# Kernel tuning notes

Measured on AMD Instinct MI355X. Metric: run time of the kernel, lower is better.

## Reference

```python
import jax, jax.numpy as jnp
import numpy as np

MAX_SEQ_LENGTH = 32
LN_EPS = 1e-5


def setup_inputs() -> dict:
    key = jax.random.key(0)
    ks = jax.random.split(key, 6)
    N, T, D, H, O = 256, 1024, 128, 256, 128
    G = 4 * H
    # torch kaiming_normal_ on a 2D (in, 4H) tensor: fan_in = size(1) = 4H, std = sqrt(2/fan_in)
    std_k = float(np.sqrt(2.0 / G))
    X = jax.random.normal(ks[0], (N, T, D), dtype=jnp.float32)
    Wx = jax.random.normal(ks[1], (D, G), dtype=jnp.float32) * std_k
    Wh = jax.random.normal(ks[2], (H, G), dtype=jnp.float32) * std_k
    b = jnp.zeros((G,), dtype=jnp.float32)
    W1 = jax.random.normal(ks[3], (H, H), dtype=jnp.float32) * float(np.sqrt(1.0 / H))
    b1 = jnp.zeros((H,), dtype=jnp.float32)
    ln_gamma = jnp.ones((H,), dtype=jnp.float32)
    ln_beta = jnp.zeros((H,), dtype=jnp.float32)
    W2 = jax.random.normal(ks[4], (H, O), dtype=jnp.float32) * float(np.sqrt(1.0 / H))
    b2 = jnp.zeros((O,), dtype=jnp.float32)
    return {"X": X, "Wx": Wx, "Wh": Wh, "b": b, "W1": W1, "b1": b1,
            "ln_gamma": ln_gamma, "ln_beta": ln_beta, "W2": W2, "b2": b2}


def _fc(h, W1, b1, ln_gamma, ln_beta, W2, b2):
    z = h @ W1 + b1
    mu = jnp.mean(z, axis=-1, keepdims=True)
    var = jnp.var(z, axis=-1, keepdims=True)
    z = (z - mu) * jax.lax.rsqrt(var + LN_EPS) * ln_gamma + ln_beta
    z = jax.nn.relu(z)
    return z @ W2 + b2


def reference(X, Wx, Wh, b, W1, b1, ln_gamma, ln_beta, W2, b2):
    N, T, D = X.shape
    H = Wh.shape[0]
    h0 = jnp.zeros((N, H), dtype=X.dtype)
    c0 = jnp.zeros((N, H), dtype=X.dtype)

    # --- encoder: standard LSTM cell (sigmoid/tanh gates) ---
    def enc_step(carry, x_t):
        h, c = carry
        fm = x_t @ Wx + h @ Wh + b  # (N, 4H)
        i = jax.nn.sigmoid(fm[:, 0:H])
        f = jax.nn.sigmoid(fm[:, H:2 * H])
        o = jax.nn.sigmoid(fm[:, 2 * H:3 * H])
        g = jnp.tanh(fm[:, 3 * H:4 * H])
        c = c * f + i * g
        h = o * jnp.tanh(c)
        return (h, c), None

    (h, c), _ = jax.lax.scan(enc_step, (h0, c0), jnp.swapaxes(X, 0, 1))

    # --- decoder: NOTE original code uses RAW gate slices (no sigmoid/tanh),
    # and start_token is zeros so the start_token @ Wx term is exactly 0. ---
    def dec_step(carry, _):
        h, c = carry
        fm = h @ Wh + b  # zeros @ Wx contributes 0
        i = fm[:, 0:H]
        f = fm[:, H:2 * H]
        o = fm[:, 2 * H:3 * H]
        g = fm[:, 3 * H:4 * H]
        c = c * f + i * g
        h = o * jnp.tanh(c)
        y = _fc(h, W1, b1, ln_gamma, ln_beta, W2, b2)
        return (h, c), y

    _, ys = jax.lax.scan(dec_step, (h, c), None, length=MAX_SEQ_LENGTH)
    return jnp.swapaxes(ys, 0, 1)  # (N, max_seq_length, output_dim)
```

## Files before the change

kernel.cpp:

```cpp
#include <hip/hip_runtime.h>
#include <cmath>

typedef _Float16 f16;
typedef _Float16 f16x4v __attribute__((ext_vector_type(4)));
typedef _Float16 f16x8v __attribute__((ext_vector_type(8)));
typedef float f32x4v __attribute__((ext_vector_type(4)));

#define NTHR 256
#define WPG  16

__device__ __forceinline__ float sigmoidf_(float x) { return 1.0f / (1.0f + expf(-x)); }

__device__ __forceinline__ void store_sc(float* p, float v) {
  asm volatile("global_store_dword %0, %1, off sc0 sc1" :: "v"(p), "v"(v) : "memory");
}

__device__ __forceinline__ void ld4_sc(const float* p,
                                       float4& a, float4& b, float4& c, float4& d) {
  asm volatile(
      "global_load_dwordx4 %0, %4, off sc0 sc1\n\t"
      "global_load_dwordx4 %1, %5, off sc0 sc1\n\t"
      "global_load_dwordx4 %2, %6, off sc0 sc1\n\t"
      "global_load_dwordx4 %3, %7, off sc0 sc1\n\t"
      "s_waitcnt vmcnt(0)"
      : "=&v"(a), "=&v"(b), "=&v"(c), "=&v"(d)
      : "v"(p), "v"(p + 1024), "v"(p + 2048), "v"(p + 3072)
      : "memory");
}

__device__ __forceinline__ void arrive_bar(unsigned* cg) {
  asm volatile("s_waitcnt vmcnt(0)" ::: "memory");
  __syncthreads();
  if (threadIdx.x == 0)
    (void)__hip_atomic_fetch_add(cg, 1u, __ATOMIC_RELAXED, __HIP_MEMORY_SCOPE_AGENT);
}

__device__ __forceinline__ void wait_bar(unsigned* cg, unsigned target) {
  if (threadIdx.x == 0) {
    unsigned guard = 0;
    while (__hip_atomic_load(cg, __ATOMIC_RELAXED, __HIP_MEMORY_SCOPE_AGENT) < target) {
      __builtin_amdgcn_s_sleep(1);
      if (++guard > (1u << 22)) break;
    }
  }
  __syncthreads();
}

__device__ __forceinline__ void conv4_wr(float4 v, f16* ph, f16* pl) {
  f16x4v h, l;
  h[0] = (f16)v.x; h[1] = (f16)v.y; h[2] = (f16)v.z; h[3] = (f16)v.w;
  l[0] = (f16)(v.x - (float)h[0]); l[1] = (f16)(v.y - (float)h[1]);
  l[2] = (f16)(v.z - (float)h[2]); l[3] = (f16)(v.w - (float)h[3]);
  *(f16x4v*)ph = h; *(f16x4v*)pl = l;
}

__device__ __forceinline__ void conv8_wr(float4 a, float4 b, f16* ph, f16* pl) {
  f16x8v h, l;
  h[0]=(f16)a.x; h[1]=(f16)a.y; h[2]=(f16)a.z; h[3]=(f16)a.w;
  h[4]=(f16)b.x; h[5]=(f16)b.y; h[6]=(f16)b.z; h[7]=(f16)b.w;
  l[0]=(f16)(a.x-(float)h[0]); l[1]=(f16)(a.y-(float)h[1]);
  l[2]=(f16)(a.z-(float)h[2]); l[3]=(f16)(a.w-(float)h[3]);
  l[4]=(f16)(b.x-(float)h[4]); l[5]=(f16)(b.y-(float)h[5]);
  l[6]=(f16)(b.z-(float)h[6]); l[7]=(f16)(b.w-(float)h[7]);
  *(f16x8v*)ph = h; *(f16x8v*)pl = l;
}

__global__ __launch_bounds__(NTHR, 1) void lstm_k(
    const float* __restrict__ X,  const float* __restrict__ Wx,
    const float* __restrict__ Wh, const float* __restrict__ Bg,
    const float* __restrict__ W1, const float* __restrict__ B1,
    const float* __restrict__ LNG, const float* __restrict__ LNB,
    const float* __restrict__ W2, const float* __restrict__ B2,
    float* __restrict__ Y, unsigned* __restrict__ CNT,
    float* __restrict__ hbuf, float* __restrict__ zbuf)
{
  __shared__ f16   A_hi[16][392];
  __shared__ f16   A_lo[16][392];
  __shared__ float fm_lds[16][65];
  __shared__ float hst[16][264];
  __shared__ float w1_lds[16][268];
  __shared__ float w2_lds[8][268];
  __shared__ float lng_lds[256], lnb_lds[256];
  __shared__ float ln_mu[16], ln_rs[16];

  const int tid = threadIdx.x;
  const int wg  = blockIdx.x;
  const int g   = wg & 15;
  const int jm  = wg >> 4;
  const int n0  = g * 16;
  const int k0  = jm * 16;
  unsigned* cg  = CNT + g * 32;

  const int l     = tid & 63;
  const int w     = __builtin_amdgcn_readfirstlane(tid >> 6);
  const int krow0 = (l >> 4) * 8;
  const int arow  = l & 15;

  f16x8v Bh[12], Bl[12];
  {
    const int bcol = w * 256 + k0 + (l & 15);
    #pragma unroll
    for (int kt = 0; kt < 12; ++kt) {
      #pragma unroll
      for (int j = 0; j < 8; ++j) {
        int k = kt * 32 + krow0 + j;
        float v = (kt < 4) ? Wx[k * 1024 + bcol] : Wh[(k - 128) * 1024 + bcol];
        f16 hi = (f16)v;
        Bh[kt][j] = hi;
        Bl[kt][j] = (f16)(v - (float)hi);
      }
    }
  }

  for (int idx = tid; idx < 256 * 16; idx += NTHR) {
    int k = idx >> 4, cc = idx & 15;
    w1_lds[cc][k] = W1[k * 256 + k0 + cc];
  }
  for (int idx = tid; idx < 256 * 8; idx += NTHR) {
    int k = idx >> 3, cc = idx & 7;
    w2_lds[cc][k] = W2[k * 128 + jm * 8 + cc];
  }
  lng_lds[tid] = LNG[tid];
  lnb_lds[tid] = LNB[tid];

  const int gr = tid >> 4, gk = tid & 15;
  const float bias0 = Bg[      k0 + gk];
  const float bias1 = Bg[256 + k0 + gk];
  const float bias2 = Bg[512 + k0 + gk];
  const float bias3 = Bg[768 + k0 + gk];
  const float b1reg = B1[k0 + gk];
  const float b2reg = (tid < 128) ? B2[jm * 8 + (tid & 7)] : 0.0f;
  float c_reg = 0.0f;

  {
    const float* xp = X + (size_t)(n0 + (tid >> 4)) * 131072 + (size_t)(tid & 15) * 8;
    float4 xa = *(const float4*)xp;
    float4 xb = *(const float4*)(xp + 4);
    conv8_wr(xa, xb, &A_hi[tid >> 4][(tid & 15) * 8], &A_lo[tid >> 4][(tid & 15) * 8]);
    f16x8v z8 = {0,0,0,0,0,0,0,0};
    *(f16x8v*)&A_hi[tid >> 4][128 + (tid & 15) * 16] = z8;
    *(f16x8v*)&A_hi[tid >> 4][136 + (tid & 15) * 16] = z8;
    *(f16x8v*)&A_lo[tid >> 4][128 + (tid & 15) * 16] = z8;
    *(f16x8v*)&A_lo[tid >> 4][136 + (tid & 15) * 16] = z8;
  }
  __syncthreads();

  auto stage_h_A = [&](const float* hs) {
    float4 v0, v1, v2, v3;
    ld4_sc(hs, v0, v1, v2, v3);
    conv4_wr(v0, &A_hi[w     ][128 + 4 * l], &A_lo[w     ][128 + 4 * l]);
    conv4_wr(v1, &A_hi[w + 4 ][128 + 4 * l], &A_lo[w + 4 ][128 + 4 * l]);
    conv4_wr(v2, &A_hi[w + 8 ][128 + 4 * l], &A_lo[w + 8 ][128 + 4 * l]);
    conv4_wr(v3, &A_hi[w + 12][128 + 4 * l], &A_lo[w + 12][128 + 4 * l]);
  };

  for (int t = 0; t < 1024; ++t) {
    float4 xa, xb;
    if (t < 1023) {
      const float* xp = X + (size_t)(n0 + (tid >> 4)) * 131072
                          + (size_t)(t + 1) * 128 + (size_t)(tid & 15) * 8;
      xa = *(const float4*)xp;
      xb = *(const float4*)(xp + 4);
    }

    f16x8v ah[12], al[12];
    {
      const f16* pah = &A_hi[arow][krow0];
      const f16* pal = &A_lo[arow][krow0];
      #pragma unroll
      for (int kt = 0; kt < 12; ++kt) {
        ah[kt] = *(const f16x8v*)(pah + kt * 32);
        al[kt] = *(const f16x8v*)(pal + kt * 32);
      }
    }
    f32x4v ac0 = {0,0,0,0}, ac1 = {0,0,0,0}, ac2 = {0,0,0,0};
    #pragma unroll
    for (int kt = 0; kt < 12; ++kt) {
      ac0 = __builtin_amdgcn_mfma_f32_16x16x32_f16(ah[kt], Bh[kt], ac0, 0, 0, 0);
      ac1 = __builtin_amdgcn_mfma_f32_16x16x32_f16(ah[kt], Bl[kt], ac1, 0, 0, 0);
      ac2 = __builtin_amdgcn_mfma_f32_16x16x32_f16(al[kt], Bh[kt], ac2, 0, 0, 0);
    }
    #pragma unroll
    for (int q = 0; q < 4; ++q)
      fm_lds[(l >> 4) * 4 + q][w * 16 + (l & 15)] = ac0[q] + ac1[q] + ac2[q];
    __syncthreads();

    {
      float fi = fm_lds[gr][     gk] + bias0;
      float ff = fm_lds[gr][16 + gk] + bias1;
      float fo = fm_lds[gr][32 + gk] + bias2;
      float fg = fm_lds[gr][48 + gk] + bias3;
      float si = sigmoidf_(fi), sf = sigmoidf_(ff), so = sigmoidf_(fo);
      float tg = tanhf(fg);
      c_reg = c_reg * sf + si * tg;
      float hv = so * tanhf(c_reg);
      store_sc(hbuf + (size_t)(t & 1) * 65536 + (size_t)(n0 + gr) * 256 + k0 + gk, hv);
    }

    if (t < 1023)
      conv8_wr(xa, xb, &A_hi[tid >> 4][(tid & 15) * 8], &A_lo[tid >> 4][(tid & 15) * 8]);

    arrive_bar(cg);
    if (t < 1023) {
      wait_bar(cg, (unsigned)(WPG * (t + 1)));
      stage_h_A(hbuf + (size_t)(t & 1) * 65536 + (size_t)n0 * 256 + (size_t)tid * 4);
      __syncthreads();
    }
  }

  wait_bar(cg, (unsigned)(WPG * 1024));
  stage_h_A(hbuf + (size_t)65536  + (size_t)n0 * 256 + (size_t)tid * 4);
  __syncthreads();
  unsigned arr = 1024;

  for (int s = 0; s < 32; ++s) {
    const int t = 1024 + s;

    f16x8v ah[8], al[8];
    {
      const f16* pah = &A_hi[arow][128 + krow0];
      const f16* pal = &A_lo[arow][128 + krow0];
      #pragma unroll
      for (int kt = 0; kt < 8; ++kt) {
        ah[kt] = *(const f16x8v*)(pah + kt * 32);
        al[kt] = *(const f16x8v*)(pal + kt * 32);
      }
    }
    f32x4v ac0 = {0,0,0,0}, ac1 = {0,0,0,0}, ac2 = {0,0,0,0};
    #pragma unroll
    for (int kt = 0; kt < 8; ++kt) {
      ac0 = __builtin_amdgcn_mfma_f32_16x16x32_f16(ah[kt], Bh[kt + 4], ac0, 0, 0, 0);
      ac1 = __builtin_amdgcn_mfma_f32_16x16x32_f16(ah[kt], Bl[kt + 4], ac1, 0, 0, 0);
      ac2 = __builtin_amdgcn_mfma_f32_16x16x32_f16(al[kt], Bh[kt + 4], ac2, 0, 0, 0);
    }
    #pragma unroll
    for (int q = 0; q < 4; ++q)
      fm_lds[(l >> 4) * 4 + q][w * 16 + (l & 15)] = ac0[q] + ac1[q] + ac2[q];
    __syncthreads();

    {
      float fi = fm_lds[gr][     gk] + bias0;
      float ff = fm_lds[gr][16 + gk] + bias1;
      float fo = fm_lds[gr][32 + gk] + bias2;
      float fg = fm_lds[gr][48 + gk] + bias3;
      c_reg = c_reg * ff + fi * fg;
      float hv = fo * tanhf(c_reg);
      store_sc(hbuf + (size_t)(t & 1) * 65536 + (size_t)(n0 + gr) * 256 + k0 + gk, hv);
    }
    arrive_bar(cg); ++arr;
    wait_bar(cg, WPG * arr);

    {
      const float* hs = hbuf + (size_t)(t & 1) * 65536 + (size_t)n0 * 256 + (size_t)tid * 4;
      float4 v0, v1, v2, v3;
      ld4_sc(hs, v0, v1, v2, v3);
      *(float4*)&hst[w     ][4 * l] = v0;
      *(float4*)&hst[w + 4 ][4 * l] = v1;
      *(float4*)&hst[w + 8 ][4 * l] = v2;
      *(float4*)&hst[w + 12][4 * l] = v3;
      conv4_wr(v0, &A_hi[w     ][128 + 4 * l], &A_lo[w     ][128 + 4 * l]);
      conv4_wr(v1, &A_hi[w + 4 ][128 + 4 * l], &A_lo[w + 4 ][128 + 4 * l]);
      conv4_wr(v2, &A_hi[w + 8 ][128 + 4 * l], &A_lo[w + 8 ][128 + 4 * l]);
      conv4_wr(v3, &A_hi[w + 12][128 + 4 * l], &A_lo[w + 12][128 + 4 * l]);
    }
    __syncthreads();

    {
      float za = b1reg;
      const float* hr = &hst[gr][0];
      const float* wr = &w1_lds[gk][0];
      #pragma unroll 4
      for (int kc = 0; kc < 64; ++kc) {
        float4 h4 = *(const float4*)(hr + kc * 4);
        float4 w4 = *(const float4*)(wr + kc * 4);
        za = fmaf(h4.x, w4.x, fmaf(h4.y, w4.y, fmaf(h4.z, w4.z, fmaf(h4.w, w4.w, za))));
      }
      store_sc(zbuf + (size_t)(n0 + gr) * 256 + k0 + gk, za);
    }
    arrive_bar(cg); ++arr;
    wait_bar(cg, WPG * arr);

    {
      const float* zs = zbuf + (size_t)n0 * 256 + (size_t)tid * 4;
      float4 v0, v1, v2, v3;
      ld4_sc(zs, v0, v1, v2, v3);
      *(float4*)&hst[w     ][4 * l] = v0;
      *(float4*)&hst[w + 4 ][4 * l] = v1;
      *(float4*)&hst[w + 8 ][4 * l] = v2;
      *(float4*)&hst[w + 12][4 * l] = v3;
    }
    __syncthreads();

    {
      const float* zr = &hst[gr][0];
      float s1 = 0.f, s2 = 0.f;
      #pragma unroll
      for (int u = 0; u < 16; ++u) { float v = zr[gk * 16 + u]; s1 += v; s2 += v * v; }
      #pragma unroll
      for (int d = 1; d < 16; d <<= 1) { s1 += __shfl_xor(s1, d); s2 += __shfl_xor(s2, d); }
      float mu = s1 * (1.0f / 256.0f);
      float var = s2 * (1.0f / 256.0f) - mu * mu;
      float rstd = rsqrtf(var + 1e-5f);
      if (gk == 0) { ln_mu[gr] = mu; ln_rs[gr] = rstd; }
    }
    __syncthreads();

    #pragma unroll
    for (int rep = 0; rep < 4; ++rep) {
      int f = tid + 256 * rep, r = f >> 6, kq = f & 63;
      float mu = ln_mu[r], rs = ln_rs[r];
      float4 v = *(float4*)&hst[r][kq * 4];
      int cb = kq * 4;
      v.x = fmaxf(fmaf((v.x - mu) * rs, lng_lds[cb    ], lnb_lds[cb    ]), 0.f);
      v.y = fmaxf(fmaf((v.y - mu) * rs, lng_lds[cb + 1], lnb_lds[cb + 1]), 0.f);
      v.z = fmaxf(fmaf((v.z - mu) * rs, lng_lds[cb + 2], lnb_lds[cb + 2]), 0.f);
      v.w = fmaxf(fmaf((v.w - mu) * rs, lng_lds[cb + 3], lnb_lds[cb + 3]), 0.f);
      *(float4*)&hst[r][kq * 4] = v;
    }
    __syncthreads();

    if (tid < 128) {
      int r = tid >> 3, yc = tid & 7;
      float ya = b2reg;
      const float* zr = &hst[r][0];
      const float* wr = &w2_lds[yc][0];
      #pragma unroll 4
      for (int kc = 0; kc < 64; ++kc) {
        float4 z4 = *(const float4*)(zr + kc * 4);
        float4 w4 = *(const float4*)(wr + kc * 4);
        ya = fmaf(z4.x, w4.x, fmaf(z4.y, w4.y, fmaf(z4.z, w4.z, fmaf(z4.w, w4.w, ya))));
      }
      Y[(size_t)(n0 + r) * 4096 + (size_t)s * 128 + jm * 8 + yc] = ya;
    }
  }
}

extern "C" void kernel_launch(void* const* d_in, const int* in_sizes, int n_in,
                              void* d_out, int out_size, void* d_ws, size_t ws_size,
                              hipStream_t stream) {
  const float* X   = (const float*)d_in[0];
  const float* Wx  = (const float*)d_in[1];
  const float* Wh  = (const float*)d_in[2];
  const float* b   = (const float*)d_in[3];
  const float* W1  = (const float*)d_in[4];
  const float* b1  = (const float*)d_in[5];
  const float* lng = (const float*)d_in[6];
  const float* lnb = (const float*)d_in[7];
  const float* W2  = (const float*)d_in[8];
  const float* b2  = (const float*)d_in[9];
  float* Y = (float*)d_out;

  unsigned* cnt = (unsigned*)d_ws;
  float* hbuf = (float*)((char*)d_ws + 2048);
  float* zbuf = hbuf + 2 * 256 * 256;
  (void)in_sizes; (void)n_in; (void)out_size; (void)ws_size;

  hipMemsetAsync(d_ws, 0, 2048, stream);
  hipLaunchKernelGGL(lstm_k, dim3(256), dim3(NTHR), 0, stream,
                     X, Wx, Wh, b, W1, b1, lng, lnb, W2, b2, Y, cnt, hbuf, zbuf);
}
```

Measured before the change: 2.964 ms.

## Interleave two batch groups per workgroup and split K across waves

Each workgroup now serves two 16-row batch groups with 8 hidden columns each, and 32 workgroups share a pair of counters. Group A's gate compute and barrier arrival run before group B's compute, so one group's cross-workgroup barrier latency can overlap the other group's work. Each wave now handles a slice of K for both gate tiles instead of the full K for one gate, which shortens each wave's serial MFMA chain; partial sums are reduced through LDS. The hidden state is exchanged as packed fp16 hi/lo words, so readers no longer re-split it. The trade-off is a barrier spanning twice as many workgroups, an extra LDS reduction, and more barrier waits per step.

```diff
diff --git a/kernel.cpp b/kernel.cpp
--- a/kernel.cpp
+++ b/kernel.cpp
@@ -2,21 +2,23 @@
 #include <cmath>
 
 typedef _Float16 f16;
-typedef _Float16 f16x4v __attribute__((ext_vector_type(4)));
 typedef _Float16 f16x8v __attribute__((ext_vector_type(8)));
 typedef float f32x4v __attribute__((ext_vector_type(4)));
 
 #define NTHR 256
-#define WPG  16
+#define WPP  32
 
 __device__ __forceinline__ float sigmoidf_(float x) { return 1.0f / (1.0f + expf(-x)); }
 
-__device__ __forceinline__ void store_sc(float* p, float v) {
+__device__ __forceinline__ void st_sc_u(unsigned* p, unsigned v) {
   asm volatile("global_store_dword %0, %1, off sc0 sc1" :: "v"(p), "v"(v) : "memory");
 }
-
-__device__ __forceinline__ void ld4_sc(const float* p,
-                                       float4& a, float4& b, float4& c, float4& d) {
+__device__ __forceinline__ void st_sc_f(float* p, float v) {
+  asm volatile("global_store_dword %0, %1, off sc0 sc1" :: "v"(p), "v"(v) : "memory");
+}
+
+__device__ __forceinline__ void ld4u_sc(const unsigned* p, uint4& a, uint4& b,
+                                        uint4& c, uint4& d) {
   asm volatile(
       "global_load_dwordx4 %0, %4, off sc0 sc1\n\t"
       "global_load_dwordx4 %1, %5, off sc0 sc1\n\t"
@@ -24,8 +26,18 @@
       "global_load_dwordx4 %3, %7, off sc0 sc1\n\t"
       "s_waitcnt vmcnt(0)"
       : "=&v"(a), "=&v"(b), "=&v"(c), "=&v"(d)
-      : "v"(p), "v"(p + 1024), "v"(p + 2048), "v"(p + 3072)
-      : "memory");
+      : "v"(p), "v"(p + 1024), "v"(p + 2048), "v"(p + 3072) : "memory");
+}
+__device__ __forceinline__ void ld4f_sc(const float* p, float4& a, float4& b,
+                                        float4& c, float4& d) {
+  asm volatile(
+      "global_load_dwordx4 %0, %4, off sc0 sc1\n\t"
+      "global_load_dwordx4 %1, %5, off sc0 sc1\n\t"
+      "global_load_dwordx4 %2, %6, off sc0 sc1\n\t"
+      "global_load_dwordx4 %3, %7, off sc0 sc1\n\t"
+      "s_waitcnt vmcnt(0)"
+      : "=&v"(a), "=&v"(b), "=&v"(c), "=&v"(d)
+      : "v"(p), "v"(p + 1024), "v"(p + 2048), "v"(p + 3072) : "memory");
 }
 
 __device__ __forceinline__ void arrive_bar(unsigned* cg) {
@@ -34,7 +46,6 @@
   if (threadIdx.x == 0)
     (void)__hip_atomic_fetch_add(cg, 1u, __ATOMIC_RELAXED, __HIP_MEMORY_SCOPE_AGENT);
 }
-
 __device__ __forceinline__ void wait_bar(unsigned* cg, unsigned target) {
   if (threadIdx.x == 0) {
     unsigned guard = 0;
@@ -46,12 +57,26 @@
   __syncthreads();
 }
 
-__device__ __forceinline__ void conv4_wr(float4 v, f16* ph, f16* pl) {
-  f16x4v h, l;
-  h[0] = (f16)v.x; h[1] = (f16)v.y; h[2] = (f16)v.z; h[3] = (f16)v.w;
-  l[0] = (f16)(v.x - (float)h[0]); l[1] = (f16)(v.y - (float)h[1]);
-  l[2] = (f16)(v.z - (float)h[2]); l[3] = (f16)(v.w - (float)h[3]);
-  *(f16x4v*)ph = h; *(f16x4v*)pl = l;
+__device__ __forceinline__ unsigned packhl(float v) {
+  f16 h = (f16)v;
+  f16 lo = (f16)(v - (float)h);
+  unsigned short hb, lb;
+  __builtin_memcpy(&hb, &h, 2); __builtin_memcpy(&lb, &lo, 2);
+  return (unsigned)hb | ((unsigned)lb << 16);
+}
+__device__ __forceinline__ float unpackf(unsigned u) {
+  unsigned short hb = (unsigned short)(u & 0xffffu), lb = (unsigned short)(u >> 16);
+  f16 h, l;
+  __builtin_memcpy(&h, &hb, 2); __builtin_memcpy(&l, &lb, 2);
+  return (float)h + (float)l;
+}
+__device__ __forceinline__ void unpack_wr(uint4 c, f16* ph, f16* pl) {
+  unsigned h01 = (c.x & 0xffffu) | (c.y << 16);
+  unsigned h23 = (c.z & 0xffffu) | (c.w << 16);
+  unsigned l01 = (c.x >> 16) | (c.y & 0xffff0000u);
+  unsigned l23 = (c.z >> 16) | (c.w & 0xffff0000u);
+  uint2 hh = {h01, h23}, ll = {l01, l23};
+  *(uint2*)ph = hh; *(uint2*)pl = ll;
 }
 
 __device__ __forceinline__ void conv8_wr(float4 a, float4 b, f16* ph, f16* pl) {
@@ -72,257 +97,333 @@
     const float* __restrict__ LNG, const float* __restrict__ LNB,
     const float* __restrict__ W2, const float* __restrict__ B2,
     float* __restrict__ Y, unsigned* __restrict__ CNT,
-    float* __restrict__ hbuf, float* __restrict__ zbuf)
+    unsigned* __restrict__ HBu, float* __restrict__ ZB)
 {
-  __shared__ f16   A_hi[16][392];
-  __shared__ f16   A_lo[16][392];
-  __shared__ float fm_lds[16][65];
-  __shared__ float hst[16][264];
-  __shared__ float w1_lds[16][268];
-  __shared__ float w2_lds[8][268];
+  __shared__ f16   A_hi[2][16][392];
+  __shared__ f16   A_lo[2][16][392];
+  __shared__ float fm_p[4][2][16][20];
+  __shared__ float hst[2][16][260];
+  __shared__ float w1_lds[8][260];
+  __shared__ float w2_lds[4][260];
   __shared__ float lng_lds[256], lnb_lds[256];
-  __shared__ float ln_mu[16], ln_rs[16];
-
-  const int tid = threadIdx.x;
-  const int wg  = blockIdx.x;
-  const int g   = wg & 15;
-  const int jm  = wg >> 4;
-  const int n0  = g * 16;
-  const int k0  = jm * 16;
-  unsigned* cg  = CNT + g * 32;
-
-  const int l     = tid & 63;
-  const int w     = __builtin_amdgcn_readfirstlane(tid >> 6);
-  const int krow0 = (l >> 4) * 8;
-  const int arow  = l & 15;
-
-  f16x8v Bh[12], Bl[12];
-  {
-    const int bcol = w * 256 + k0 + (l & 15);
-    #pragma unroll
-    for (int kt = 0; kt < 12; ++kt) {
+  __shared__ float ln_mu[2][16], ln_rs[2][16];
+
+  const int tid  = threadIdx.x;
+  const int wg   = blockIdx.x;
+  const int pair = wg >> 5;
+  const int jm   = wg & 31;
+  const int n0A  = pair * 32;
+  const int n0B  = n0A + 16;
+  unsigned* cgA  = CNT + (2 * pair)     * 32;
+  unsigned* cgB  = CNT + (2 * pair + 1) * 32;
+
+  const int l  = tid & 63;
+  const int wv = __builtin_amdgcn_readfirstlane(tid >> 6);
+  const int lr = l & 15;
+  const int ko = (l >> 4) * 8;
+
+  f16x8v Bh[3][2], Bl[3][2];
+  #pragma unroll
+  for (int ki = 0; ki < 3; ++ki) {
+    const int kt = wv + 4 * ki;
+    #pragma unroll
+    for (int n = 0; n < 2; ++n) {
+      const int gq  = 2 * n + (lr >> 3);
+      const int col = gq * 256 + 8 * jm + (lr & 7);
       #pragma unroll
       for (int j = 0; j < 8; ++j) {
-        int k = kt * 32 + krow0 + j;
-        float v = (kt < 4) ? Wx[k * 1024 + bcol] : Wh[(k - 128) * 1024 + bcol];
+        int k = kt * 32 + ko + j;
+        float v = (k < 128) ? Wx[k * 1024 + col] : Wh[(k - 128) * 1024 + col];
         f16 hi = (f16)v;
-        Bh[kt][j] = hi;
-        Bl[kt][j] = (f16)(v - (float)hi);
+        Bh[ki][n][j] = hi;
+        Bl[ki][n][j] = (f16)(v - (float)hi);
       }
     }
   }
 
-  for (int idx = tid; idx < 256 * 16; idx += NTHR) {
-    int k = idx >> 4, cc = idx & 15;
-    w1_lds[cc][k] = W1[k * 256 + k0 + cc];
-  }
   for (int idx = tid; idx < 256 * 8; idx += NTHR) {
-    int k = idx >> 3, cc = idx & 7;
-    w2_lds[cc][k] = W2[k * 128 + jm * 8 + cc];
+    int k = idx >> 3, c = idx & 7;
+    w1_lds[c][k] = W1[k * 256 + 8 * jm + c];
+  }
+  for (int idx = tid; idx < 256 * 4; idx += NTHR) {
+    int k = idx >> 2, c = idx & 3;
+    w2_lds[c][k] = W2[k * 128 + 4 * jm + c];
   }
   lng_lds[tid] = LNG[tid];
   lnb_lds[tid] = LNB[tid];
 
-  const int gr = tid >> 4, gk = tid & 15;
-  const float bias0 = Bg[      k0 + gk];
-  const float bias1 = Bg[256 + k0 + gk];
-  const float bias2 = Bg[512 + k0 + gk];
-  const float bias3 = Bg[768 + k0 + gk];
-  const float b1reg = B1[k0 + gk];
-  const float b2reg = (tid < 128) ? B2[jm * 8 + (tid & 7)] : 0.0f;
+  const int r_g = (tid & 127) >> 3;
+  const int c8  = tid & 7;
+  const float bias0 = Bg[        8 * jm + c8];
+  const float bias1 = Bg[256   + 8 * jm + c8];
+  const float bias2 = Bg[512   + 8 * jm + c8];
+  const float bias3 = Bg[768   + 8 * jm + c8];
+  const float b1reg = B1[8 * jm + c8];
+  const float b2reg = B2[4 * jm + (tid & 3)];
   float c_reg = 0.0f;
 
   {
-    const float* xp = X + (size_t)(n0 + (tid >> 4)) * 131072 + (size_t)(tid & 15) * 8;
-    float4 xa = *(const float4*)xp;
-    float4 xb = *(const float4*)(xp + 4);
-    conv8_wr(xa, xb, &A_hi[tid >> 4][(tid & 15) * 8], &A_lo[tid >> 4][(tid & 15) * 8]);
+    const int row = tid >> 4, cb = (tid & 15) * 16;
     f16x8v z8 = {0,0,0,0,0,0,0,0};
-    *(f16x8v*)&A_hi[tid >> 4][128 + (tid & 15) * 16] = z8;
-    *(f16x8v*)&A_hi[tid >> 4][136 + (tid & 15) * 16] = z8;
-    *(f16x8v*)&A_lo[tid >> 4][128 + (tid & 15) * 16] = z8;
-    *(f16x8v*)&A_lo[tid >> 4][136 + (tid & 15) * 16] = z8;
+    #pragma unroll
+    for (int g2 = 0; g2 < 2; ++g2) {
+      *(f16x8v*)&A_hi[g2][row][128 + cb]     = z8;
+      *(f16x8v*)&A_hi[g2][row][128 + cb + 8] = z8;
+      *(f16x8v*)&A_lo[g2][row][128 + cb]     = z8;
+      *(f16x8v*)&A_lo[g2][row][128 + cb + 8] = z8;
+    }
+    const float* xpA = X + (size_t)(n0A + row) * 131072 + (size_t)(tid & 15) * 8;
+    conv8_wr(*(const float4*)xpA, *(const float4*)(xpA + 4),
+             &A_hi[0][row][(tid & 15) * 8], &A_lo[0][row][(tid & 15) * 8]);
+    const float* xpB = xpA + (size_t)16 * 131072;
+    conv8_wr(*(const float4*)xpB, *(const float4*)(xpB + 4),
+             &A_hi[1][row][(tid & 15) * 8], &A_lo[1][row][(tid & 15) * 8]);
   }
   __syncthreads();
 
-  auto stage_h_A = [&](const float* hs) {
-    float4 v0, v1, v2, v3;
-    ld4_sc(hs, v0, v1, v2, v3);
-    conv4_wr(v0, &A_hi[w     ][128 + 4 * l], &A_lo[w     ][128 + 4 * l]);
-    conv4_wr(v1, &A_hi[w + 4 ][128 + 4 * l], &A_lo[w + 4 ][128 + 4 * l]);
-    conv4_wr(v2, &A_hi[w + 8 ][128 + 4 * l], &A_lo[w + 8 ][128 + 4 * l]);
-    conv4_wr(v3, &A_hi[w + 12][128 + 4 * l], &A_lo[w + 12][128 + 4 * l]);
+  auto stage_h = [&](const unsigned* base, int g2) {
+    uint4 c0, c1, c2, c3;
+    ld4u_sc(base + tid * 4, c0, c1, c2, c3);
+    const int r0 = tid >> 6, cb = (tid & 63) * 4;
+    unpack_wr(c0, &A_hi[g2][r0     ][128 + cb], &A_lo[g2][r0     ][128 + cb]);
+    unpack_wr(c1, &A_hi[g2][r0 + 4 ][128 + cb], &A_lo[g2][r0 + 4 ][128 + cb]);
+    unpack_wr(c2, &A_hi[g2][r0 + 8 ][128 + cb], &A_lo[g2][r0 + 8 ][128 + cb]);
+    unpack_wr(c3, &A_hi[g2][r0 + 12][128 + cb], &A_lo[g2][r0 + 12][128 + cb]);
   };
+  auto stage_h_hst = [&](const unsigned* base, int g2) {
+    uint4 c0, c1, c2, c3;
+    ld4u_sc(base + tid * 4, c0, c1, c2, c3);
+    const int r0 = tid >> 6, cb = (tid & 63) * 4;
+    unpack_wr(c0, &A_hi[g2][r0     ][128 + cb], &A_lo[g2][r0     ][128 + cb]);
+    unpack_wr(c1, &A_hi[g2][r0 + 4 ][128 + cb], &A_lo[g2][r0 + 4 ][128 + cb]);
+    unpack_wr(c2, &A_hi[g2][r0 + 8 ][128 + cb], &A_lo[g2][r0 + 8 ][128 + cb]);
+    unpack_wr(c3, &A_hi[g2][r0 + 12][128 + cb], &A_lo[g2][r0 + 12][128 + cb]);
+    float4 f0 = {unpackf(c0.x), unpackf(c0.y), unpackf(c0.z), unpackf(c0.w)};
+    float4 f1 = {unpackf(c1.x), unpackf(c1.y), unpackf(c1.z), unpackf(c1.w)};
+    float4 f2 = {unpackf(c2.x), unpackf(c2.y), unpackf(c2.z), unpackf(c2.w)};
+    float4 f3 = {unpackf(c3.x), unpackf(c3.y), unpackf(c3.z), unpackf(c3.w)};
+    *(float4*)&hst[g2][r0     ][cb] = f0;
+    *(float4*)&hst[g2][r0 + 4 ][cb] = f1;
+    *(float4*)&hst[g2][r0 + 8 ][cb] = f2;
+    *(float4*)&hst[g2][r0 + 12][cb] = f3;
+  };
+
+  auto fm_compute = [&](int g2, bool with_x) {
+    f32x4v a0[2], a1[2], a2[2];
+    #pragma unroll
+    for (int n = 0; n < 2; ++n) { a0[n] = {0,0,0,0}; a1[n] = {0,0,0,0}; a2[n] = {0,0,0,0}; }
+    f16x8v ah1 = *(const f16x8v*)&A_hi[g2][lr][128 + wv * 32 + ko];
+    f16x8v al1 = *(const f16x8v*)&A_lo[g2][lr][128 + wv * 32 + ko];
+    f16x8v ah2 = *(const f16x8v*)&A_hi[g2][lr][128 + (wv + 4) * 32 + ko];
+    f16x8v al2 = *(const f16x8v*)&A_lo[g2][lr][128 + (wv + 4) * 32 + ko];
+    if (with_x) {
+      f16x8v axh = *(const f16x8v*)&A_hi[g2][lr][wv * 32 + ko];
+      f16x8v axl = *(const f16x8v*)&A_lo[g2][lr][wv * 32 + ko];
+      #pragma unroll
+      for (int n = 0; n < 2; ++n) {
+        a0[n] = __builtin_amdgcn_mfma_f32_16x16x32_f16(axh, Bh[0][n], a0[n], 0, 0, 0);
+        a1[n] = __builtin_amdgcn_mfma_f32_16x16x32_f16(axh, Bl[0][n], a1[n], 0, 0, 0);
+        a2[n] = __builtin_amdgcn_mfma_f32_16x16x32_f16(axl, Bh[0][n], a2[n], 0, 0, 0);
+      }
+    }
+    #pragma unroll
+    for (int n = 0; n < 2; ++n) {
+      a0[n] = __builtin_amdgcn_mfma_f32_16x16x32_f16(ah1, Bh[1][n], a0[n], 0, 0, 0);
+      a1[n] = __builtin_amdgcn_mfma_f32_16x16x32_f16(ah1, Bl[1][n], a1[n], 0, 0, 0);
+      a2[n] = __builtin_amdgcn_mfma_f32_16x16x32_f16(al1, Bh[1][n], a2[n], 0, 0, 0);
+      a0[n] = __builtin_amdgcn_mfma_f32_16x16x32_f16(ah2, Bh[2][n], a0[n], 0, 0, 0);
+      a1[n] = __builtin_amdgcn_mfma_f32_16x16x32_f16(ah2, Bl[2][n], a1[n], 0, 0, 0);
+      a2[n] = __builtin_amdgcn_mfma_f32_16x16x32_f16(al2, Bh[2][n], a2[n], 0, 0, 0);
+    }
+    #pragma unroll
+    for (int n = 0; n < 2; ++n) {
+      f32x4v sm = a0[n] + a1[n] + a2[n];
+      *(f32x4v*)&fm_p[wv][n][lr][(l >> 4) * 4] = sm;
+    }
+  };
+
+  auto reduce4 = [&](float& fi, float& ff, float& fo, float& fg) {
+    fi = bias0; ff = bias1; fo = bias2; fg = bias3;
+    #pragma unroll
+    for (int ww = 0; ww < 4; ++ww) {
+      fi += fm_p[ww][0][c8][r_g];
+      ff += fm_p[ww][0][8 + c8][r_g];
+      fo += fm_p[ww][1][c8][r_g];
+      fg += fm_p[ww][1][8 + c8][r_g];
+    }
+  };
+
+  const size_t HBUF = 65536;
 
   for (int t = 0; t < 1024; ++t) {
-    float4 xa, xb;
+    float4 xaA, xbA, xaB, xbB;
     if (t < 1023) {
-      const float* xp = X + (size_t)(n0 + (tid >> 4)) * 131072
-                          + (size_t)(t + 1) * 128 + (size_t)(tid & 15) * 8;
-      xa = *(const float4*)xp;
-      xb = *(const float4*)(xp + 4);
-    }
-
-    f16x8v ah[12], al[12];
-    {
-      const f16* pah = &A_hi[arow][krow0];
-      const f16* pal = &A_lo[arow][krow0];
-      #pragma unroll
-      for (int kt = 0; kt < 12; ++kt) {
-        ah[kt] = *(const f16x8v*)(pah + kt * 32);
-        al[kt] = *(const f16x8v*)(pal + kt * 32);
-      }
-    }
-    f32x4v ac0 = {0,0,0,0}, ac1 = {0,0,0,0}, ac2 = {0,0,0,0};
-    #pragma unroll
-    for (int kt = 0; kt < 12; ++kt) {
-      ac0 = __builtin_amdgcn_mfma_f32_16x16x32_f16(ah[kt], Bh[kt], ac0, 0, 0, 0);
-      ac1 = __builtin_amdgcn_mfma_f32_16x16x32_f16(ah[kt], Bl[kt], ac1, 0, 0, 0);
-      ac2 = __builtin_amdgcn_mfma_f32_16x16x32_f16(al[kt], Bh[kt], ac2, 0, 0, 0);
-    }
-    #pragma unroll
-    for (int q = 0; q < 4; ++q)
-      fm_lds[(l >> 4) * 4 + q][w * 16 + (l & 15)] = ac0[q] + ac1[q] + ac2[q];
-    __syncthreads();
-
-    {
-      float fi = fm_lds[gr][     gk] + bias0;
-      float ff = fm_lds[gr][16 + gk] + bias1;
-      float fo = fm_lds[gr][32 + gk] + bias2;
-      float fg = fm_lds[gr][48 + gk] + bias3;
+      const float* xpA = X + (size_t)(n0A + (tid >> 4)) * 131072
+                           + (size_t)(t + 1) * 128 + (size_t)(tid & 15) * 8;
+      xaA = *(const float4*)xpA; xbA = *(const float4*)(xpA + 4);
+      const float* xpB = xpA + (size_t)16 * 131072;
+      xaB = *(const float4*)xpB; xbB = *(const float4*)(xpB + 4);
+    }
+
+    fm_compute(0, true);
+    __syncthreads();
+    if (tid < 128) {
+      float fi, ff, fo, fg; reduce4(fi, ff, fo, fg);
       float si = sigmoidf_(fi), sf = sigmoidf_(ff), so = sigmoidf_(fo);
       float tg = tanhf(fg);
       c_reg = c_reg * sf + si * tg;
       float hv = so * tanhf(c_reg);
-      store_sc(hbuf + (size_t)(t & 1) * 65536 + (size_t)(n0 + gr) * 256 + k0 + gk, hv);
-    }
-
+      st_sc_u(HBu + (size_t)(t & 1) * HBUF + (size_t)(n0A + r_g) * 256 + 8 * jm + c8,
+              packhl(hv));
+    }
     if (t < 1023)
-      conv8_wr(xa, xb, &A_hi[tid >> 4][(tid & 15) * 8], &A_lo[tid >> 4][(tid & 15) * 8]);
-
-    arrive_bar(cg);
+      conv8_wr(xaA, xbA, &A_hi[0][tid >> 4][(tid & 15) * 8],
+                         &A_lo[0][tid >> 4][(tid & 15) * 8]);
+    arrive_bar(cgA);
+
+    fm_compute(1, true);
+    __syncthreads();
+    if (tid >= 128) {
+      float fi, ff, fo, fg; reduce4(fi, ff, fo, fg);
+      float si = sigmoidf_(fi), sf = sigmoidf_(ff), so = sigmoidf_(fo);
+      float tg = tanhf(fg);
+      c_reg = c_reg * sf + si * tg;
+      float hv = so * tanhf(c_reg);
+      st_sc_u(HBu + (size_t)(t & 1) * HBUF + (size_t)(n0B + r_g) * 256 + 8 * jm + c8,
+              packhl(hv));
+    }
+    if (t < 1023)
+      conv8_wr(xaB, xbB, &A_hi[1][tid >> 4][(tid & 15) * 8],
+                         &A_lo[1][tid >> 4][(tid & 15) * 8]);
+    arrive_bar(cgB);
+
     if (t < 1023) {
-      wait_bar(cg, (unsigned)(WPG * (t + 1)));
-      stage_h_A(hbuf + (size_t)(t & 1) * 65536 + (size_t)n0 * 256 + (size_t)tid * 4);
+      wait_bar(cgA, (unsigned)(WPP * (t + 1)));
+      stage_h(HBu + (size_t)(t & 1) * HBUF + (size_t)n0A * 256, 0);
+      wait_bar(cgB, (unsigned)(WPP * (t + 1)));
+      stage_h(HBu + (size_t)(t & 1) * HBUF + (size_t)n0B * 256, 1);
       __syncthreads();
     }
   }
 
-  wait_bar(cg, (unsigned)(WPG * 1024));
-  stage_h_A(hbuf + (size_t)65536  + (size_t)n0 * 256 + (size_t)tid * 4);
+  wait_bar(cgA, (unsigned)(WPP * 1024));
+  stage_h(HBu + HBUF + (size_t)n0A * 256, 0);
+  wait_bar(cgB, (unsigned)(WPP * 1024));
+  stage_h(HBu + HBUF + (size_t)n0B * 256, 1);
   __syncthreads();
   unsigned arr = 1024;
 
   for (int s = 0; s < 32; ++s) {
     const int t = 1024 + s;
 
-    f16x8v ah[8], al[8];
-    {
-      const f16* pah = &A_hi[arow][128 + krow0];
-      const f16* pal = &A_lo[arow][128 + krow0];
-      #pragma unroll
-      for (int kt = 0; kt < 8; ++kt) {
-        ah[kt] = *(const f16x8v*)(pah + kt * 32);
-        al[kt] = *(const f16x8v*)(pal + kt * 32);
-      }
-    }
-    f32x4v ac0 = {0,0,0,0}, ac1 = {0,0,0,0}, ac2 = {0,0,0,0};
-    #pragma unroll
-    for (int kt = 0; kt < 8; ++kt) {
-      ac0 = __builtin_amdgcn_mfma_f32_16x16x32_f16(ah[kt], Bh[kt + 4], ac0, 0, 0, 0);
-      ac1 = __builtin_amdgcn_mfma_f32_16x16x32_f16(ah[kt], Bl[kt + 4], ac1, 0, 0, 0);
-      ac2 = __builtin_amdgcn_mfma_f32_16x16x32_f16(al[kt], Bh[kt + 4], ac2, 0, 0, 0);
-    }
-    #pragma unroll
-    for (int q = 0; q < 4; ++q)
-      fm_lds[(l >> 4) * 4 + q][w * 16 + (l & 15)] = ac0[q] + ac1[q] + ac2[q];
-    __syncthreads();
-
-    {
-      float fi = fm_lds[gr][     gk] + bias0;
-      float ff = fm_lds[gr][16 + gk] + bias1;
-      float fo = fm_lds[gr][32 + gk] + bias2;
-      float fg = fm_lds[gr][48 + gk] + bias3;
+    fm_compute(0, false);
+    __syncthreads();
+    if (tid < 128) {
+      float fi, ff, fo, fg; reduce4(fi, ff, fo, fg);
       c_reg = c_reg * ff + fi * fg;
       float hv = fo * tanhf(c_reg);
-      store_sc(hbuf + (size_t)(t & 1) * 65536 + (size_t)(n0 + gr) * 256 + k0 + gk, hv);
-    }
-    arrive_bar(cg); ++arr;
-    wait_bar(cg, WPG * arr);
+      st_sc_u(HBu + (size_t)(t & 1) * HBUF + (size_t)(n0A + r_g) * 256 + 8 * jm + c8,
+              packhl(hv));
+    }
+    arrive_bar(cgA);
+
+    fm_compute(1, false);
+    __syncthreads();
+    if (tid >= 128) {
+      float fi, ff, fo, fg; reduce4(fi, ff, fo, fg);
+      c_reg = c_reg * ff + fi * fg;
+      float hv = fo * tanhf(c_reg);
+      st_sc_u(HBu + (size_t)(t & 1) * HBUF + (size_t)(n0B + r_g) * 256 + 8 * jm + c8,
+              packhl(hv));
+    }
+    arrive_bar(cgB);
+    ++arr;
+
+    wait_bar(cgA, WPP * arr);
+    stage_h_hst(HBu + (size_t)(t & 1) * HBUF + (size_t)n0A * 256, 0);
+    wait_bar(cgB, WPP * arr);
+    stage_h_hst(HBu + (size_t)(t & 1) * HBUF + (size_t)n0B * 256, 1);
+    __syncthreads();
 
     {
-      const float* hs = hbuf + (size_t)(t & 1) * 65536 + (size_t)n0 * 256 + (size_t)tid * 4;
-      float4 v0, v1, v2, v3;
-      ld4_sc(hs, v0, v1, v2, v3);
-      *(float4*)&hst[w     ][4 * l] = v0;
-      *(float4*)&hst[w + 4 ][4 * l] = v1;
-      *(float4*)&hst[w + 8 ][4 * l] = v2;
-      *(float4*)&hst[w + 12][4 * l] = v3;
-      conv4_wr(v0, &A_hi[w     ][128 + 4 * l], &A_lo[w     ][128 + 4 * l]);
-      conv4_wr(v1, &A_hi[w + 4 ][128 + 4 * l], &A_lo[w + 4 ][128 + 4 * l]);
-      conv4_wr(v2, &A_hi[w + 8 ][128 + 4 * l], &A_lo[w + 8 ][128 + 4 * l]);
-      conv4_wr(v3, &A_hi[w + 12][128 + 4 * l], &A_lo[w + 12][128 + 4 * l]);
-    }
-    __syncthreads();
-
-    {
+      const int g2 = tid >> 7;
       float za = b1reg;
-      const float* hr = &hst[gr][0];
-      const float* wr = &w1_lds[gk][0];
+      const float* hr = &hst[g2][r_g][0];
+      const float* wr = &w1_lds[c8][0];
       #pragma unroll 4
       for (int kc = 0; kc < 64; ++kc) {
         float4 h4 = *(const float4*)(hr + kc * 4);
         float4 w4 = *(const float4*)(wr + kc * 4);
         za = fmaf(h4.x, w4.x, fmaf(h4.y, w4.y, fmaf(h4.z, w4.z, fmaf(h4.w, w4.w, za))));
       }
-      store_sc(zbuf + (size_t)(n0 + gr) * 256 + k0 + gk, za);
-    }
-    arrive_bar(cg); ++arr;
-    wait_bar(cg, WPG * arr);
-
+      st_sc_f(ZB + (size_t)(n0A + g2 * 16 + r_g) * 256 + 8 * jm + c8, za);
+    }
+    asm volatile("s_waitcnt vmcnt(0)" ::: "memory");
+    __syncthreads();
+    if (tid == 0) {
+      (void)__hip_atomic_fetch_add(cgA, 1u, __ATOMIC_RELAXED, __HIP_MEMORY_SCOPE_AGENT);
+      (void)__hip_atomic_fetch_add(cgB, 1u, __ATOMIC_RELAXED, __HIP_MEMORY_SCOPE_AGENT);
+    }
+    ++arr;
+
+    wait_bar(cgA, WPP * arr);
     {
-      const float* zs = zbuf + (size_t)n0 * 256 + (size_t)tid * 4;
-      float4 v0, v1, v2, v3;
-      ld4_sc(zs, v0, v1, v2, v3);
-      *(float4*)&hst[w     ][4 * l] = v0;
-      *(float4*)&hst[w + 4 ][4 * l] = v1;
-      *(float4*)&hst[w + 8 ][4 * l] = v2;
-      *(float4*)&hst[w + 12][4 * l] = v3;
-    }
-    __syncthreads();
-
+      float4 a, b, c, d;
+      ld4f_sc(ZB + (size_t)n0A * 256 + tid * 4, a, b, c, d);
+      const int r0 = tid >> 6, cb = (tid & 63) * 4;
+      *(float4*)&hst[0][r0][cb] = a;      *(float4*)&hst[0][r0 + 4][cb] = b;
+      *(float4*)&hst[0][r0 + 8][cb] = c;  *(float4*)&hst[0][r0 + 12][cb] = d;
+    }
+    wait_bar(cgB, WPP * arr);
     {
-      const float* zr = &hst[gr][0];
+      float4 a, b, c, d;
+      ld4f_sc(ZB + (size_t)n0B * 256 + tid * 4, a, b, c, d);
+      const int r0 = tid >> 6, cb = (tid & 63) * 4;
+      *(float4*)&hst[1][r0][cb] = a;      *(float4*)&hst[1][r0 + 4][cb] = b;
+      *(float4*)&hst[1][r0 + 8][cb] = c;  *(float4*)&hst[1][r0 + 12][cb] = d;
+    }
+    __syncthreads();
+
+    {
+      const int g2 = tid >> 7;
+      const int l8 = tid & 7;
+      const float* zr = &hst[g2][r_g][0];
       float s1 = 0.f, s2 = 0.f;
       #pragma unroll
-      for (int u = 0; u < 16; ++u) { float v = zr[gk * 16 + u]; s1 += v; s2 += v * v; }
+      for (int k = 0; k < 8; ++k) {
+        float4 v = *(const float4*)(zr + l8 * 4 + k * 32);
+        s1 += v.x + v.y + v.z + v.w;
+        s2 += v.x*v.x + v.y*v.y + v.z*v.z + v.w*v.w;
+      }
       #pragma unroll
-      for (int d = 1; d < 16; d <<= 1) { s1 += __shfl_xor(s1, d); s2 += __shfl_xor(s2, d); }
+      for (int d = 1; d < 8; d <<= 1) { s1 += __shfl_xor(s1, d); s2 += __shfl_xor(s2, d); }
       float mu = s1 * (1.0f / 256.0f);
       float var = s2 * (1.0f / 256.0f) - mu * mu;
       float rstd = rsqrtf(var + 1e-5f);
-      if (gk == 0) { ln_mu[gr] = mu; ln_rs[gr] = rstd; }
-    }
-    __syncthreads();
-
-    #pragma unroll
-    for (int rep = 0; rep < 4; ++rep) {
-      int f = tid + 256 * rep, r = f >> 6, kq = f & 63;
-      float mu = ln_mu[r], rs = ln_rs[r];
-      float4 v = *(float4*)&hst[r][kq * 4];
-      int cb = kq * 4;
+      if (l8 == 0) { ln_mu[g2][r_g] = mu; ln_rs[g2][r_g] = rstd; }
+    }
+    __syncthreads();
+
+    #pragma unroll
+    for (int rep = 0; rep < 8; ++rep) {
+      int idx = tid + 256 * rep;
+      int g2 = idx >> 10, r = (idx >> 6) & 15, q = idx & 63;
+      float mu = ln_mu[g2][r], rs = ln_rs[g2][r];
+      float4 v = *(float4*)&hst[g2][r][q * 4];
+      int cb = q * 4;
       v.x = fmaxf(fmaf((v.x - mu) * rs, lng_lds[cb    ], lnb_lds[cb    ]), 0.f);
       v.y = fmaxf(fmaf((v.y - mu) * rs, lng_lds[cb + 1], lnb_lds[cb + 1]), 0.f);
       v.z = fmaxf(fmaf((v.z - mu) * rs, lng_lds[cb + 2], lnb_lds[cb + 2]), 0.f);
       v.w = fmaxf(fmaf((v.w - mu) * rs, lng_lds[cb + 3], lnb_lds[cb + 3]), 0.f);
-      *(float4*)&hst[r][kq * 4] = v;
-    }
-    __syncthreads();
-
-    if (tid < 128) {
-      int r = tid >> 3, yc = tid & 7;
+      *(float4*)&hst[g2][r][q * 4] = v;
+    }
+    __syncthreads();
+
+    if ((tid & 127) < 64) {
+      const int g2 = tid >> 7;
+      const int r = (tid & 63) >> 2, yc = tid & 3;
       float ya = b2reg;
-      const float* zr = &hst[r][0];
+      const float* zr = &hst[g2][r][0];
       const float* wr = &w2_lds[yc][0];
       #pragma unroll 4
       for (int kc = 0; kc < 64; ++kc) {
@@ -330,8 +431,9 @@
         float4 w4 = *(const float4*)(wr + kc * 4);
         ya = fmaf(z4.x, w4.x, fmaf(z4.y, w4.y, fmaf(z4.z, w4.z, fmaf(z4.w, w4.w, ya))));
       }
-      Y[(size_t)(n0 + r) * 4096 + (size_t)s * 128 + jm * 8 + yc] = ya;
-    }
+      Y[(size_t)(n0A + g2 * 16 + r) * 4096 + (size_t)s * 128 + 4 * jm + yc] = ya;
+    }
+    __syncthreads();
   }
 }
 
@@ -350,12 +452,12 @@
   const float* b2  = (const float*)d_in[9];
   float* Y = (float*)d_out;
 
-  unsigned* cnt = (unsigned*)d_ws;
-  float* hbuf = (float*)((char*)d_ws + 2048);
-  float* zbuf = hbuf + 2 * 256 * 256;
+  unsigned* CNTp = (unsigned*)d_ws;
+  unsigned* HBu  = (unsigned*)((char*)d_ws + 4096);
+  float*    ZB   = (float*)((char*)d_ws + 4096 + 524288);
   (void)in_sizes; (void)n_in; (void)out_size; (void)ws_size;
 
   hipMemsetAsync(d_ws, 0, 2048, stream);
   hipLaunchKernelGGL(lstm_k, dim3(256), dim3(NTHR), 0, stream,
-                     X, Wx, Wh, b, W1, b1, lng, lnb, W2, b2, Y, cnt, hbuf, zbuf);
-}
+                     X, Wx, Wh, b, W1, b1, lng, lnb, W2, b2, Y, CNTp, HBu, ZB);
+}
```

New measurement: 4.716 ms. 1.59x slower.
